# Performance work log

Hardware: AMD Instinct MI355X
Metric: run time of the kernel (lower is better)

The kernel has to match this reference:

```python
import jax, jax.numpy as jnp
import numpy as np

D_OUT, D1, D2 = 512, 512, 512
R0, R1, R2 = 128, 128, 128
BATCH = 8192


def setup_inputs() -> dict:
    key = jax.random.key(0)
    k1, k2, k3, k4, k5, k6 = jax.random.split(key, 6)
    return {
        "X1": jax.random.normal(k1, (D1, BATCH), dtype=jnp.float32),
        "X2": jax.random.normal(k2, (D2, BATCH), dtype=jnp.float32),
        "U0": jax.random.normal(k3, (D_OUT, R0), dtype=jnp.float32) * 0.05,
        "U1": jax.random.normal(k4, (D1, R1), dtype=jnp.float32) * 0.05,
        "U2": jax.random.normal(k5, (D2, R2), dtype=jnp.float32) * 0.05,
        "G": jax.random.normal(k6, (R0, R1, R2), dtype=jnp.float32) * 0.05,
    }


def reference(X1, X2, U0, U1, U2, G):
    # Per-mode projections: UX_i = U_{i+1}^T @ X_i  -> [r_i, B]
    UX1 = U1.T @ X1  # [R1, B]
    UX2 = U2.T @ X2  # [R2, B]
    # Column-wise Khatri-Rao product of UX1, UX2 gives kron per column with
    # row index q*R2 + r (C order), which matches mode-0 unfolding of G.
    # Fused form: core = G_(0) @ khatri_rao(UX1, UX2), expressed as one einsum.
    core = jnp.einsum('pqr,qb,rb->pb', G, UX1, UX2)  # [R0, B]
    Z = U0 @ core  # [D_OUT, B]
    return Z
```

## Files before the change

### kernel.cpp

```cpp
#include <hip/hip_runtime.h>
#include <hip/hip_bf16.h>
#include <stdint.h>


typedef __attribute__((ext_vector_type(8))) short bf8;
typedef __attribute__((ext_vector_type(4))) short bf4;
typedef __attribute__((ext_vector_type(4))) float f4;

__device__ __forceinline__ unsigned short f2bf(float f){
  unsigned x = __builtin_bit_cast(unsigned, f);
  x += 0x7fffu + ((x >> 16) & 1u);
  return (unsigned short)(x >> 16);
}
__device__ __forceinline__ float bf2f(unsigned short u){
  unsigned x = ((unsigned)u) << 16;
  return __builtin_bit_cast(float, x);
}
__device__ __forceinline__ void glds16(const void* g, void* l){
  __builtin_amdgcn_global_load_lds(
      (const __attribute__((address_space(1))) void*)g,
      (__attribute__((address_space(3))) void*)l, 16, 0, 0);
}

__global__ __launch_bounds__(256) void k_cast(const float* __restrict__ G,
                                              const float* __restrict__ U0,
                                              const float* __restrict__ U1,
                                              const float* __restrict__ U2,
                                              unsigned short* __restrict__ Gbf,
                                              unsigned short* __restrict__ U0bf,
                                              unsigned short* __restrict__ U1T,
                                              unsigned short* __restrict__ U2T){
  const int blk = blockIdx.x;
  if (blk < 2112){
    const int i4 = blk * 256 + threadIdx.x;
    const int NG4 = 2097152 / 4;
    const float4* src; unsigned short* dst; int j4;
    if (i4 < NG4){ src = (const float4*)G;  dst = Gbf;  j4 = i4; }
    else         { src = (const float4*)U0; dst = U0bf; j4 = i4 - NG4; }
    float4 v = src[j4];
    ushort4 o = make_ushort4(f2bf(v.x), f2bf(v.y), f2bf(v.z), f2bf(v.w));
    ((ushort4*)dst)[j4] = o;
  } else {
    const int b2 = blk - 2112;
    const float* U = (b2 < 256) ? U1 : U2;
    unsigned short* UT = (b2 < 256) ? U1T : U2T;
    const int idx = (b2 & 255) * 256 + threadIdx.x;
    const int d = idx >> 7, q = idx & 127;
    UT[q * 512 + d] = f2bf(U[idx]);
  }
}

__global__ __launch_bounds__(256) void k_ux2(const unsigned short* __restrict__ U1T,
                                             const unsigned short* __restrict__ U2T,
                                             const float* __restrict__ X1,
                                             const float* __restrict__ X2,
                                             float* __restrict__ OUTF,
                                             unsigned short* __restrict__ OUTT){
  const bool second = (blockIdx.y != 0);
  const unsigned short* UT = second ? U2T : U1T;
  const float* X = second ? X2 : X1;
  __shared__ __align__(16) unsigned char lds[16384 + 8192];
  unsigned char* ldsA = lds;
  unsigned char* ldsB = lds + 16384;
  const int tid = threadIdx.x, lane = tid & 63, wv = tid >> 6;
  const int wr = wv >> 1, wc = wv & 1;
  const int b0 = blockIdx.x * 64;
  f4 acc[4][2] = {};

  for (int it = 0; it < 8; ++it){
    const int k0 = it * 64;
#pragma unroll
    for (int i = 0; i < 4; ++i){
      const int L = (wv * 4 + i) * 1024 + lane * 16;
      const int row = L >> 7;
      const int ss = (lane & 7) ^ (row & 7);
      glds16(UT + (size_t)row * 512 + k0 + ss * 8, ldsA + (wv * 4 + i) * 1024);
    }
#pragma unroll
    for (int c = 0; c < 2; ++c){
      const int slot = c * 4 + wv;
      const int bRow = lane;
      bf8 v;
#pragma unroll
      for (int j = 0; j < 8; ++j)
        v[j] = (short)f2bf(X[(size_t)(k0 + slot * 8 + j) * 8192 + b0 + bRow]);
      *(bf8*)(ldsB + bRow * 128 + ((slot ^ (bRow & 7)) << 4)) = v;
    }
    __syncthreads();
#pragma unroll
    for (int kc = 0; kc < 2; ++kc){
      const int g = lane >> 4;
      bf8 a[4], b[2];
#pragma unroll
      for (int mf = 0; mf < 4; ++mf){
        const int r = wr * 64 + mf * 16 + (lane & 15);
        a[mf] = *(const bf8*)(ldsA + r * 128 + (((kc * 4 + g) ^ (r & 7)) << 4));
      }
#pragma unroll
      for (int nf = 0; nf < 2; ++nf){
        const int rb = wc * 32 + nf * 16 + (lane & 15);
        b[nf] = *(const bf8*)(ldsB + rb * 128 + (((kc * 4 + g) ^ (rb & 7)) << 4));
      }
#pragma unroll
      for (int mf = 0; mf < 4; ++mf)
#pragma unroll
        for (int nf = 0; nf < 2; ++nf)
          acc[mf][nf] = __builtin_amdgcn_mfma_f32_16x16x32_bf16(a[mf], b[nf], acc[mf][nf], 0, 0, 0);
    }
    __syncthreads();
  }

  if (!second){
#pragma unroll
    for (int mf = 0; mf < 4; ++mf)
#pragma unroll
      for (int nf = 0; nf < 2; ++nf)
#pragma unroll
        for (int j = 0; j < 4; ++j){
          const int q = wr * 64 + mf * 16 + (lane >> 4) * 4 + j;
          const int b = b0 + wc * 32 + nf * 16 + (lane & 15);
          OUTF[(size_t)q * 8192 + b] = acc[mf][nf][j];
        }
  } else {
#pragma unroll
    for (int mf = 0; mf < 4; ++mf)
#pragma unroll
      for (int nf = 0; nf < 2; ++nf){
        const int rBase = wr * 64 + mf * 16 + (lane >> 4) * 4;
        const int bL = wc * 32 + nf * 16 + (lane & 15);
        bf4 p;
#pragma unroll
        for (int j = 0; j < 4; ++j) p[j] = (short)f2bf(acc[mf][nf][j]);
        *(bf4*)(lds + ((bL * 256 + rBase * 2) ^ ((bL & 7) << 4))) = p;
      }
    __syncthreads();
#pragma unroll
    for (int u = 0; u < 4; ++u){
      const int sIdx = u * 256 + tid;
      const int bL = sIdx >> 4, slot = sIdx & 15;
      bf8 v = *(const bf8*)(lds + bL * 256 + ((slot ^ (bL & 7)) << 4));
      *(bf8*)(OUTT + (size_t)(b0 + bL) * 128 + slot * 8) = v;
    }
  }
}

__global__ __launch_bounds__(512, 2) void k_core(const unsigned short* __restrict__ Gbf,
                                                 const float* __restrict__ UX1,
                                                 const unsigned short* __restrict__ UX2T,
                                                 float* __restrict__ PT){
  __shared__ __align__(16) unsigned char lds[65536];
  const int tid = threadIdx.x, lane = tid & 63, wv = tid >> 6;
  const int g = lane >> 4, l15 = lane & 15;
  const int blk = blockIdx.x;
  const int xcd = blk & 7, slot = blk >> 3;
  const int split = xcd >> 1;
  const int bblk = (xcd & 1) * 32 + slot;
  const int b0 = bblk * 128;
  const int q0 = split * 32;
  const int p0 = wv * 16;

  f4 acc[8] = {(f4){0,0,0,0}};
#pragma unroll
  for (int nf = 0; nf < 8; ++nf) acc[nf] = (f4){0.f, 0.f, 0.f, 0.f};

#pragma unroll
  for (int h = 0; h < 2; ++h){
    bf8 Bf[2][8];
#pragma unroll
    for (int kc = 0; kc < 2; ++kc)
#pragma unroll
      for (int nf = 0; nf < 8; ++nf)
        Bf[kc][nf] = *(const bf8*)(UX2T + (size_t)(b0 + nf * 16 + l15) * 128 +
                                   h * 64 + kc * 32 + g * 8);
    const unsigned short* ap = Gbf + (size_t)(p0 + l15) * 16384 + q0 * 128 + h * 64 + g * 8;
    const float* xp = UX1 + (size_t)q0 * 8192 + b0 + l15;

    bf8 a0 = *(const bf8*)(ap);
    bf8 a1 = *(const bf8*)(ap + 32);
    float xs[8];
#pragma unroll
    for (int nf = 0; nf < 8; ++nf) xs[nf] = xp[nf * 16];

    for (int i = 0; i < 31; ++i){
      bf8 n0 = *(const bf8*)(ap + (i + 1) * 128);
      bf8 n1 = *(const bf8*)(ap + (i + 1) * 128 + 32);
      float xn[8];
#pragma unroll
      for (int nf = 0; nf < 8; ++nf) xn[nf] = xp[(size_t)(i + 1) * 8192 + nf * 16];
      f4 y[8];
#pragma unroll
      for (int nf = 0; nf < 8; ++nf)
        y[nf] = __builtin_amdgcn_mfma_f32_16x16x32_bf16(a0, Bf[0][nf], (f4){0.f,0.f,0.f,0.f}, 0, 0, 0);
#pragma unroll
      for (int nf = 0; nf < 8; ++nf)
        y[nf] = __builtin_amdgcn_mfma_f32_16x16x32_bf16(a1, Bf[1][nf], y[nf], 0, 0, 0);
#pragma unroll
      for (int nf = 0; nf < 8; ++nf) acc[nf] += y[nf] * xs[nf];
      a0 = n0; a1 = n1;
#pragma unroll
      for (int nf = 0; nf < 8; ++nf) xs[nf] = xn[nf];
    }
    {
      f4 y[8];
#pragma unroll
      for (int nf = 0; nf < 8; ++nf)
        y[nf] = __builtin_amdgcn_mfma_f32_16x16x32_bf16(a0, Bf[0][nf], (f4){0.f,0.f,0.f,0.f}, 0, 0, 0);
#pragma unroll
      for (int nf = 0; nf < 8; ++nf)
        y[nf] = __builtin_amdgcn_mfma_f32_16x16x32_bf16(a1, Bf[1][nf], y[nf], 0, 0, 0);
#pragma unroll
      for (int nf = 0; nf < 8; ++nf) acc[nf] += y[nf] * xs[nf];
    }
  }

#pragma unroll
  for (int nf = 0; nf < 8; ++nf){
    const int bL = nf * 16 + l15;
    const int pq = wv * 4 + g;
    *(f4*)(lds + bL * 512 + ((pq ^ (bL & 7)) << 4)) = acc[nf];
  }
  __syncthreads();
#pragma unroll
  for (int rnd = 0; rnd < 8; ++rnd){
    const int idx = rnd * 512 + tid;
    const int bL = idx >> 5, sl = idx & 31;
    f4 v = *(const f4*)(lds + bL * 512 + ((sl ^ (bL & 7)) << 4));
    *(f4*)(PT + (size_t)split * 1048576 + (size_t)(b0 + bL) * 128 + sl * 4) = v;
  }
}

__global__ __launch_bounds__(256) void k_red(const float* __restrict__ PT,
                                             unsigned short* __restrict__ coreT){
  const int i4 = blockIdx.x * 256 + threadIdx.x;
  const f4* P = (const f4*)PT;
  f4 v = P[i4];
  v += P[262144 + i4];
  v += P[2 * 262144 + i4];
  v += P[3 * 262144 + i4];
  ushort4 o = make_ushort4(f2bf(v[0]), f2bf(v[1]), f2bf(v[2]), f2bf(v[3]));
  ((ushort4*)coreT)[i4] = o;
}

__global__ __launch_bounds__(256) void k_z(const unsigned short* __restrict__ U0bf,
                                           const unsigned short* __restrict__ coreT,
                                           float* __restrict__ Z){
  __shared__ __align__(16) unsigned char lds[32768];
  unsigned char* ldsA = lds;
  unsigned char* ldsB = lds + 16384;
  const int tid = threadIdx.x, lane = tid & 63, wv = tid >> 6;
  const int wr = wv >> 1, wc = wv & 1;
  const int b0 = blockIdx.x * 128;
  const int d0 = blockIdx.y * 128;
  f4 acc[4][4] = {};

#pragma unroll
  for (int it = 0; it < 2; ++it){
    const int k0 = it * 64;
#pragma unroll
    for (int i = 0; i < 4; ++i){
      const int L = (wv * 4 + i) * 1024 + lane * 16;
      const int row = L >> 7;
      const int ss = (lane & 7) ^ (row & 7);
      glds16(U0bf + (size_t)(d0 + row) * 128 + k0 + ss * 8, ldsA + (wv * 4 + i) * 1024);
      glds16(coreT + (size_t)(b0 + row) * 128 + k0 + ss * 8, ldsB + (wv * 4 + i) * 1024);
    }
    __syncthreads();
#pragma unroll
    for (int kc = 0; kc < 2; ++kc){
      const int g = lane >> 4;
      bf8 a[4], b[4];
#pragma unroll
      for (int mf = 0; mf < 4; ++mf){
        const int r = wr * 64 + mf * 16 + (lane & 15);
        a[mf] = *(const bf8*)(ldsA + r * 128 + (((kc * 4 + g) ^ (r & 7)) << 4));
      }
#pragma unroll
      for (int nf = 0; nf < 4; ++nf){
        const int rb = wc * 64 + nf * 16 + (lane & 15);
        b[nf] = *(const bf8*)(ldsB + rb * 128 + (((kc * 4 + g) ^ (rb & 7)) << 4));
      }
#pragma unroll
      for (int mf = 0; mf < 4; ++mf)
#pragma unroll
        for (int nf = 0; nf < 4; ++nf)
          acc[mf][nf] = __builtin_amdgcn_mfma_f32_16x16x32_bf16(a[mf], b[nf], acc[mf][nf], 0, 0, 0);
    }
    __syncthreads();
  }
#pragma unroll
  for (int mf = 0; mf < 4; ++mf)
#pragma unroll
    for (int nf = 0; nf < 4; ++nf)
#pragma unroll
      for (int j = 0; j < 4; ++j){
        const int d = d0 + wr * 64 + mf * 16 + (lane >> 4) * 4 + j;
        const int b = b0 + wc * 64 + nf * 16 + (lane & 15);
        Z[(size_t)d * 8192 + b] = acc[mf][nf][j];
      }
}

extern "C" void kernel_launch(void* const* d_in, const int* in_sizes, int n_in,
                              void* d_out, int out_size, void* d_ws, size_t ws_size,
                              hipStream_t stream){
  const float* X1 = (const float*)d_in[0];
  const float* X2 = (const float*)d_in[1];
  const float* U0 = (const float*)d_in[2];
  const float* U1 = (const float*)d_in[3];
  const float* U2 = (const float*)d_in[4];
  const float* G  = (const float*)d_in[5];
  float* Z = (float*)d_out;

  char* ws = (char*)d_ws;
  unsigned short* Gbf   = (unsigned short*)(ws);
  unsigned short* U0bf  = (unsigned short*)(ws + 4194304);
  unsigned short* U1T   = (unsigned short*)(ws + 4325376);
  unsigned short* U2T   = (unsigned short*)(ws + 4456448);
  float*          UX1   = (float*)         (ws + 4587520);
  unsigned short* UX2T  = (unsigned short*)(ws + 8781824);
  unsigned short* coreT = (unsigned short*)(ws + 10878976);
  float*          PT    = (float*)         (ws + 12976128);

  k_cast<<<dim3(2624), dim3(256), 0, stream>>>(G, U0, U1, U2, Gbf, U0bf, U1T, U2T);
  k_ux2 <<<dim3(128, 2), dim3(256), 0, stream>>>(U1T, U2T, X1, X2, UX1, UX2T);
  k_core<<<dim3(256), dim3(512), 0, stream>>>(Gbf, UX1, UX2T, PT);
  k_red <<<dim3(1024), dim3(256), 0, stream>>>(PT, coreT);
  k_z   <<<dim3(64, 4), dim3(256), 0, stream>>>(U0bf, coreT, Z);
}
```

Measured before the change: 82.16 us.

## Stage G slices through a 4-deep LDS ring and store partials as bf16

The core contraction kernel now streams each G q-slice into a four-buffer LDS ring with async global-to-LDS loads, waiting on vmcnt before each step. Waves are rearranged into a 4x2 grid so each wave reuses 32 rows of A against 64 batch columns, with full-K B fragments kept in registers. UX1 is also preloaded into LDS. This targets the redundant per-wave global loads of G and the load latency in the old loop. Split-K partials are written as bf16 instead of fp32, which halves the traffic into the reduction kernel. The cost is 144KB of LDS per block, which may limit occupancy to one block per CU despite launch_bounds(512,2), plus extra rounding error in the partial sums.

```diff
diff --git a/kernel.cpp b/kernel.cpp
--- a/kernel.cpp
+++ b/kernel.cpp
@@ -147,98 +147,130 @@
 __global__ __launch_bounds__(512, 2) void k_core(const unsigned short* __restrict__ Gbf,
                                                  const float* __restrict__ UX1,
                                                  const unsigned short* __restrict__ UX2T,
-                                                 float* __restrict__ PT){
-  __shared__ __align__(16) unsigned char lds[65536];
+                                                 unsigned short* __restrict__ PT){
+  __shared__ __align__(16) unsigned char lds[147456];
+  unsigned char* ldsX = lds + 131072;
   const int tid = threadIdx.x, lane = tid & 63, wv = tid >> 6;
   const int g = lane >> 4, l15 = lane & 15;
+  const int wr = wv >> 1, wc = wv & 1;
   const int blk = blockIdx.x;
   const int xcd = blk & 7, slot = blk >> 3;
   const int split = xcd >> 1;
-  const int bblk = (xcd & 1) * 32 + slot;
-  const int b0 = bblk * 128;
+  const int b0 = ((xcd & 1) * 32 + slot) * 128;
   const int q0 = split * 32;
-  const int p0 = wv * 16;
-
-  f4 acc[8] = {(f4){0,0,0,0}};
-#pragma unroll
-  for (int nf = 0; nf < 8; ++nf) acc[nf] = (f4){0.f, 0.f, 0.f, 0.f};
-
-#pragma unroll
-  for (int h = 0; h < 2; ++h){
-    bf8 Bf[2][8];
-#pragma unroll
-    for (int kc = 0; kc < 2; ++kc)
-#pragma unroll
-      for (int nf = 0; nf < 8; ++nf)
-        Bf[kc][nf] = *(const bf8*)(UX2T + (size_t)(b0 + nf * 16 + l15) * 128 +
-                                   h * 64 + kc * 32 + g * 8);
-    const unsigned short* ap = Gbf + (size_t)(p0 + l15) * 16384 + q0 * 128 + h * 64 + g * 8;
-    const float* xp = UX1 + (size_t)q0 * 8192 + b0 + l15;
-
-    bf8 a0 = *(const bf8*)(ap);
-    bf8 a1 = *(const bf8*)(ap + 32);
-    float xs[8];
-#pragma unroll
-    for (int nf = 0; nf < 8; ++nf) xs[nf] = xp[nf * 16];
-
-    for (int i = 0; i < 31; ++i){
-      bf8 n0 = *(const bf8*)(ap + (i + 1) * 128);
-      bf8 n1 = *(const bf8*)(ap + (i + 1) * 128 + 32);
-      float xn[8];
-#pragma unroll
-      for (int nf = 0; nf < 8; ++nf) xn[nf] = xp[(size_t)(i + 1) * 8192 + nf * 16];
-      f4 y[8];
-#pragma unroll
-      for (int nf = 0; nf < 8; ++nf)
-        y[nf] = __builtin_amdgcn_mfma_f32_16x16x32_bf16(a0, Bf[0][nf], (f4){0.f,0.f,0.f,0.f}, 0, 0, 0);
-#pragma unroll
-      for (int nf = 0; nf < 8; ++nf)
-        y[nf] = __builtin_amdgcn_mfma_f32_16x16x32_bf16(a1, Bf[1][nf], y[nf], 0, 0, 0);
-#pragma unroll
-      for (int nf = 0; nf < 8; ++nf) acc[nf] += y[nf] * xs[nf];
-      a0 = n0; a1 = n1;
-#pragma unroll
-      for (int nf = 0; nf < 8; ++nf) xs[nf] = xn[nf];
-    }
-    {
-      f4 y[8];
-#pragma unroll
-      for (int nf = 0; nf < 8; ++nf)
-        y[nf] = __builtin_amdgcn_mfma_f32_16x16x32_bf16(a0, Bf[0][nf], (f4){0.f,0.f,0.f,0.f}, 0, 0, 0);
-#pragma unroll
-      for (int nf = 0; nf < 8; ++nf)
-        y[nf] = __builtin_amdgcn_mfma_f32_16x16x32_bf16(a1, Bf[1][nf], y[nf], 0, 0, 0);
-#pragma unroll
-      for (int nf = 0; nf < 8; ++nf) acc[nf] += y[nf] * xs[nf];
-    }
-  }
-
-#pragma unroll
-  for (int nf = 0; nf < 8; ++nf){
-    const int bL = nf * 16 + l15;
-    const int pq = wv * 4 + g;
-    *(f4*)(lds + bL * 512 + ((pq ^ (bL & 7)) << 4)) = acc[nf];
-  }
+
+  auto stageA = [&](int q, int buf){
+#pragma unroll
+    for (int rnd = 0; rnd < 4; ++rnd){
+      const int off = rnd * 8192 + wv * 1024 + lane * 16;
+      const int row = off >> 8;
+      const int ss = ((off >> 4) & 15) ^ (row & 7);
+      glds16(Gbf + (size_t)row * 16384 + (size_t)q * 128 + ss * 8,
+             lds + buf * 32768 + off);
+    }
+  };
+
+#pragma unroll
+  for (int rnd = 0; rnd < 2; ++rnd){
+    const int off = rnd * 8192 + wv * 1024 + lane * 16;
+    const int row = off >> 9;
+    glds16(UX1 + (size_t)(q0 + row) * 8192 + b0 + ((off >> 2) & 127), ldsX + off);
+  }
+  bf8 Bf[4][4];
+#pragma unroll
+  for (int kc = 0; kc < 4; ++kc)
+#pragma unroll
+    for (int nf = 0; nf < 4; ++nf)
+      Bf[kc][nf] = *(const bf8*)(UX2T + (size_t)(b0 + wc * 64 + nf * 16 + l15) * 128 +
+                                 kc * 32 + g * 8);
+  stageA(q0 + 0, 0);
+  stageA(q0 + 1, 1);
+  stageA(q0 + 2, 2);
+
+  f4 acc[2][4];
+#pragma unroll
+  for (int mf = 0; mf < 2; ++mf)
+#pragma unroll
+    for (int nf = 0; nf < 4; ++nf) acc[mf][nf] = (f4){0.f, 0.f, 0.f, 0.f};
+
+  auto bodyq = [&](int i){
+    const unsigned char* A = lds + (i & 3) * 32768;
+    float xs[4];
+#pragma unroll
+    for (int nf = 0; nf < 4; ++nf)
+      xs[nf] = *(const float*)(ldsX + i * 512 + (wc * 64 + nf * 16 + l15) * 4);
+    bf8 a[2][4];
+#pragma unroll
+    for (int mf = 0; mf < 2; ++mf){
+      const int row = wr * 32 + mf * 16 + l15;
+#pragma unroll
+      for (int kc = 0; kc < 4; ++kc)
+        a[mf][kc] = *(const bf8*)(A + row * 256 + ((((kc << 2) + g) ^ (row & 7)) << 4));
+    }
+#pragma unroll
+    for (int mf = 0; mf < 2; ++mf)
+#pragma unroll
+      for (int nf = 0; nf < 4; ++nf){
+        f4 y = __builtin_amdgcn_mfma_f32_16x16x32_bf16(a[mf][0], Bf[0][nf], (f4){0.f,0.f,0.f,0.f}, 0, 0, 0);
+        y = __builtin_amdgcn_mfma_f32_16x16x32_bf16(a[mf][1], Bf[1][nf], y, 0, 0, 0);
+        y = __builtin_amdgcn_mfma_f32_16x16x32_bf16(a[mf][2], Bf[2][nf], y, 0, 0, 0);
+        y = __builtin_amdgcn_mfma_f32_16x16x32_bf16(a[mf][3], Bf[3][nf], y, 0, 0, 0);
+        acc[mf][nf] += y * xs[nf];
+      }
+  };
+
+  for (int i = 0; i < 30; ++i){
+    asm volatile("s_waitcnt vmcnt(8)" ::: "memory");
+    __builtin_amdgcn_s_barrier();
+    stageA(q0 + i + 3, (i + 3) & 3);
+    bodyq(i);
+  }
+  asm volatile("s_waitcnt vmcnt(4)" ::: "memory");
+  __builtin_amdgcn_s_barrier();
+  bodyq(30);
+  asm volatile("s_waitcnt vmcnt(0)" ::: "memory");
+  __builtin_amdgcn_s_barrier();
+  bodyq(31);
+
   __syncthreads();
 #pragma unroll
-  for (int rnd = 0; rnd < 8; ++rnd){
+  for (int mf = 0; mf < 2; ++mf)
+#pragma unroll
+    for (int nf = 0; nf < 4; ++nf){
+      const int bL = wc * 64 + nf * 16 + l15;
+      const int pq = wr * 8 + mf * 4 + g;
+      *(f4*)(lds + bL * 512 + ((pq ^ (bL & 7)) << 4)) = acc[mf][nf];
+    }
+  __syncthreads();
+#pragma unroll
+  for (int rnd = 0; rnd < 4; ++rnd){
     const int idx = rnd * 512 + tid;
-    const int bL = idx >> 5, sl = idx & 31;
-    f4 v = *(const f4*)(lds + bL * 512 + ((sl ^ (bL & 7)) << 4));
-    *(f4*)(PT + (size_t)split * 1048576 + (size_t)(b0 + bL) * 128 + sl * 4) = v;
-  }
-}
-
-__global__ __launch_bounds__(256) void k_red(const float* __restrict__ PT,
+    const int bL = idx >> 4, s8 = idx & 15;
+    f4 lo = *(const f4*)(lds + bL * 512 + (((s8 * 2) ^ (bL & 7)) << 4));
+    f4 hi = *(const f4*)(lds + bL * 512 + (((s8 * 2 + 1) ^ (bL & 7)) << 4));
+    bf8 o;
+#pragma unroll
+    for (int j = 0; j < 4; ++j){
+      o[j] = (short)f2bf(lo[j]);
+      o[4 + j] = (short)f2bf(hi[j]);
+    }
+    *(bf8*)(PT + (size_t)split * 1048576 + (size_t)(b0 + bL) * 128 + s8 * 8) = o;
+  }
+}
+
+__global__ __launch_bounds__(256) void k_red(const unsigned short* __restrict__ PT,
                                              unsigned short* __restrict__ coreT){
-  const int i4 = blockIdx.x * 256 + threadIdx.x;
-  const f4* P = (const f4*)PT;
-  f4 v = P[i4];
-  v += P[262144 + i4];
-  v += P[2 * 262144 + i4];
-  v += P[3 * 262144 + i4];
-  ushort4 o = make_ushort4(f2bf(v[0]), f2bf(v[1]), f2bf(v[2]), f2bf(v[3]));
-  ((ushort4*)coreT)[i4] = o;
+  const int c = blockIdx.x * 256 + threadIdx.x;
+  const bf8* P = (const bf8*)PT;
+  bf8 v0 = P[c], v1 = P[c + 131072], v2 = P[c + 262144], v3 = P[c + 393216];
+  bf8 o;
+#pragma unroll
+  for (int j = 0; j < 8; ++j){
+    float s = bf2f((unsigned short)v0[j]) + bf2f((unsigned short)v1[j]) +
+              bf2f((unsigned short)v2[j]) + bf2f((unsigned short)v3[j]);
+    o[j] = (short)f2bf(s);
+  }
+  ((bf8*)coreT)[c] = o;
 }
 
 __global__ __launch_bounds__(256) void k_z(const unsigned short* __restrict__ U0bf,
@@ -318,11 +350,11 @@
   float*          UX1   = (float*)         (ws + 4587520);
   unsigned short* UX2T  = (unsigned short*)(ws + 8781824);
   unsigned short* coreT = (unsigned short*)(ws + 10878976);
-  float*          PT    = (float*)         (ws + 12976128);
+  unsigned short* PT    = (unsigned short*)(ws + 12976128);
 
   k_cast<<<dim3(2624), dim3(256), 0, stream>>>(G, U0, U1, U2, Gbf, U0bf, U1T, U2T);
   k_ux2 <<<dim3(128, 2), dim3(256), 0, stream>>>(U1T, U2T, X1, X2, UX1, UX2T);
   k_core<<<dim3(256), dim3(512), 0, stream>>>(Gbf, UX1, UX2T, PT);
-  k_red <<<dim3(1024), dim3(256), 0, stream>>>(PT, coreT);
+  k_red <<<dim3(512), dim3(256), 0, stream>>>(PT, coreT);
   k_z   <<<dim3(64, 4), dim3(256), 0, stream>>>(U0bf, coreT, Z);
 }
```

Result: faster. 70.06 us (-14.7%).
